# Performance work log

Hardware: AMD Instinct MI355X
Metric: run time of the kernel (lower is better)

The kernel has to match this reference:

```python
import jax, jax.numpy as jnp
import numpy as np

D_MODEL = 1024
NUM_HEADS = 16
D_K = D_MODEL // NUM_HEADS
SCALE = D_K ** 0.5


def setup_inputs() -> dict:
    key = jax.random.key(0)
    ks = jax.random.split(key, 11)
    B, S = 2, 2048
    std = 1.0 / np.sqrt(D_MODEL)
    inp = {
        "query": jax.random.normal(ks[0], (B, S, D_MODEL), dtype=jnp.float32),
        "key": jax.random.normal(ks[1], (B, S, D_MODEL), dtype=jnp.float32),
        "value": jax.random.normal(ks[2], (B, S, D_MODEL), dtype=jnp.float32),
        "wq": jax.random.uniform(ks[3], (D_MODEL, D_MODEL), jnp.float32, -std, std),
        "bq": jax.random.uniform(ks[4], (D_MODEL,), jnp.float32, -std, std),
        "wk": jax.random.uniform(ks[5], (D_MODEL, D_MODEL), jnp.float32, -std, std),
        "bk": jax.random.uniform(ks[6], (D_MODEL,), jnp.float32, -std, std),
        "wv": jax.random.uniform(ks[7], (D_MODEL, D_MODEL), jnp.float32, -std, std),
        "bv": jax.random.uniform(ks[8], (D_MODEL,), jnp.float32, -std, std),
        "wo": jax.random.uniform(ks[9], (D_MODEL, D_MODEL), jnp.float32, -std, std),
        "bo": jax.random.uniform(ks[10], (D_MODEL,), jnp.float32, -std, std),
    }
    return inp


def _split_heads(x):
    # [B, S, d_model] -> [B, H, S, d_k]
    B, S, _ = x.shape
    return x.reshape(B, S, NUM_HEADS, D_K).transpose(0, 2, 1, 3)


def reference(query, key, value, wq, bq, wk, bk, wv, bv, wo, bo):
    # Linear layers: torch Linear computes x @ W^T + b; weights here stored as [out, in]
    q = _split_heads(query @ wq.T + bq)  # [B, H, S, d_k]
    k = _split_heads(key @ wk.T + bk)
    v = _split_heads(value @ wv.T + bv)
    scores = jnp.einsum("bhqd,bhkd->bhqk", q, k) / SCALE  # [B, H, Sq, Sk]
    attn = jax.nn.softmax(scores, axis=-1)
    ctx = jnp.einsum("bhqk,bhkd->bhqd", attn, v)  # [B, H, S, d_k]
    B, H, S, dk = ctx.shape
    ctx = ctx.transpose(0, 2, 1, 3).reshape(B, S, D_MODEL)
    return ctx @ wo.T + bo
```

## Files before the change

### kernel.cpp

```cpp
#include <hip/hip_runtime.h>
#include <hip/hip_bf16.h>


typedef __attribute__((ext_vector_type(8))) short short8;
typedef __attribute__((ext_vector_type(4))) float floatx4;

#define D_MODEL 1024
#define SEQ 2048
#define NTOK 4096
#define DK 64
#define NH 16
#define MAT 4194304
#define WMAT 1048576

static __device__ __forceinline__ unsigned short f2bf(float f) {
    unsigned int x = __float_as_uint(f);
    unsigned int r = x + 0x7fffu + ((x >> 16) & 1u);
    return (unsigned short)(r >> 16);
}
static __device__ __forceinline__ float bf2f(unsigned short u) {
    return __uint_as_float(((unsigned int)u) << 16);
}
static __device__ __forceinline__ unsigned pk2(float x, float y) {
    __hip_bfloat162 h = __float22bfloat162_rn(make_float2(x, y));
    return *reinterpret_cast<unsigned*>(&h);
}
static __device__ __forceinline__ short8 cvt8(float4 f0, float4 f1) {
    union { unsigned u[4]; short8 s; } r;
    r.u[0] = pk2(f0.x, f0.y); r.u[1] = pk2(f0.z, f0.w);
    r.u[2] = pk2(f1.x, f1.y); r.u[3] = pk2(f1.z, f1.w);
    return r.s;
}

__global__ __launch_bounds__(256) void cvt7(
    const float* __restrict__ s0, const float* __restrict__ s1,
    const float* __restrict__ s2, const float* __restrict__ s3,
    const float* __restrict__ s4, const float* __restrict__ s5,
    const float* __restrict__ s6, unsigned short* __restrict__ dst) {
    const float* s; size_t doff; int n;
    switch (blockIdx.y) {
        case 0: s = s0; doff = 0;                          n = MAT;  break;
        case 1: s = s1; doff = (size_t)MAT;                n = MAT;  break;
        case 2: s = s2; doff = (size_t)2 * MAT;            n = MAT;  break;
        case 3: s = s3; doff = (size_t)3 * MAT;            n = WMAT; break;
        case 4: s = s4; doff = (size_t)3 * MAT + WMAT;     n = WMAT; break;
        case 5: s = s5; doff = (size_t)3 * MAT + 2 * WMAT; n = WMAT; break;
        default: s = s6; doff = (size_t)3 * MAT + 3 * WMAT; n = WMAT; break;
    }
    int idx = (blockIdx.x * 256 + threadIdx.x) * 8;
    if (idx >= n) return;
    float4 a = *(const float4*)(s + idx);
    float4 b = *(const float4*)(s + idx + 4);
    *(short8*)&dst[doff + idx] = cvt8(a, b);
}

template <bool F32OUT>
static __device__ __forceinline__ void gemm_bb(const unsigned short* __restrict__ X,
                                               const unsigned short* __restrict__ W,
                                               const float* __restrict__ bias,
                                               void* __restrict__ outp) {
    __shared__ __align__(16) unsigned short Asm[128 * 72];
    __shared__ __align__(16) unsigned short Bsm[128 * 72];

    const int tid = threadIdx.x;
    const int lane = tid & 63;
    const int wv = tid >> 6;
    const int g = lane >> 4;
    const int lm = lane & 15;
    const int wr = wv >> 1;
    const int wc = wv & 1;
    const int m0 = blockIdx.y * 128;
    const int n0 = blockIdx.x * 128;

    floatx4 acc[4][4];
#pragma unroll
    for (int mi = 0; mi < 4; ++mi)
#pragma unroll
        for (int ni = 0; ni < 4; ++ni)
            acc[mi][ni] = (floatx4){0.f, 0.f, 0.f, 0.f};

    for (int k0 = 0; k0 < 1024; k0 += 64) {
#pragma unroll
        for (int i = 0; i < 4; ++i) {
            int idx = tid + i * 256;
            int row = idx >> 3;
            int col = (idx & 7) << 3;
            *(uint4*)&Asm[row * 72 + col] =
                *(const uint4*)&X[(size_t)(m0 + row) * 1024 + k0 + col];
            *(uint4*)&Bsm[row * 72 + col] =
                *(const uint4*)&W[(size_t)(n0 + row) * 1024 + k0 + col];
        }
        __syncthreads();
#pragma unroll
        for (int ks = 0; ks < 64; ks += 32) {
            short8 af[4], bfr[4];
#pragma unroll
            for (int mi = 0; mi < 4; ++mi)
                af[mi] = *(const short8*)&Asm[(wr * 64 + mi * 16 + lm) * 72 + ks + g * 8];
#pragma unroll
            for (int ni = 0; ni < 4; ++ni)
                bfr[ni] = *(const short8*)&Bsm[(wc * 64 + ni * 16 + lm) * 72 + ks + g * 8];
#pragma unroll
            for (int mi = 0; mi < 4; ++mi)
#pragma unroll
                for (int ni = 0; ni < 4; ++ni)
                    acc[mi][ni] = __builtin_amdgcn_mfma_f32_16x16x32_bf16(
                        af[mi], bfr[ni], acc[mi][ni], 0, 0, 0);
        }
        __syncthreads();
    }

    float bb[4];
#pragma unroll
    for (int ni = 0; ni < 4; ++ni)
        bb[ni] = bias[n0 + wc * 64 + ni * 16 + lm];
#pragma unroll
    for (int mi = 0; mi < 4; ++mi)
#pragma unroll
        for (int ni = 0; ni < 4; ++ni)
#pragma unroll
            for (int r = 0; r < 4; ++r) {
                int rowg = m0 + wr * 64 + mi * 16 + g * 4 + r;
                int colg = n0 + wc * 64 + ni * 16 + lm;
                if (F32OUT)
                    ((float*)outp)[(size_t)rowg * 1024 + colg] = acc[mi][ni][r] + bb[ni];
                else
                    ((unsigned short*)outp)[(size_t)rowg * 1024 + colg] =
                        f2bf(acc[mi][ni][r] + bb[ni]);
            }
}

__global__ __launch_bounds__(256) void qkv_gemm_b(
    const unsigned short* __restrict__ Xb, const unsigned short* __restrict__ Wb,
    const float* __restrict__ bq, const float* __restrict__ bk,
    const float* __restrict__ bv, unsigned short* __restrict__ QKV) {
    const int z = blockIdx.z;
    const float* bias = (z == 0) ? bq : (z == 1) ? bk : bv;
    gemm_bb<false>(Xb + (size_t)z * MAT, Wb + (size_t)z * WMAT, bias,
                   QKV + (size_t)z * MAT);
}

__global__ __launch_bounds__(256) void out_gemm_b(
    const unsigned short* __restrict__ ctx, const unsigned short* __restrict__ Wo,
    const float* __restrict__ bo, float* __restrict__ out) {
    gemm_bb<true>(ctx, Wo, bo, out);
}

static __device__ __forceinline__ void gemm128_f(const float* __restrict__ X,
                                                 const float* __restrict__ W,
                                                 const float* __restrict__ bias,
                                                 unsigned short* __restrict__ out) {
    __shared__ __align__(16) unsigned short Asm[128 * 72];
    __shared__ __align__(16) unsigned short Bsm[128 * 72];
    const int tid = threadIdx.x;
    const int lane = tid & 63;
    const int wv = tid >> 6;
    const int g = lane >> 4;
    const int lm = lane & 15;
    const int wr = wv >> 1;
    const int wc = wv & 1;
    const int m0 = blockIdx.y * 128;
    const int n0 = blockIdx.x * 128;
    floatx4 acc[4][4];
#pragma unroll
    for (int mi = 0; mi < 4; ++mi)
#pragma unroll
        for (int ni = 0; ni < 4; ++ni)
            acc[mi][ni] = (floatx4){0.f, 0.f, 0.f, 0.f};
    for (int k0 = 0; k0 < 1024; k0 += 64) {
#pragma unroll
        for (int i = 0; i < 4; ++i) {
            int idx = tid + i * 256;
            int row = idx >> 3;
            int col = (idx & 7) << 3;
            const float* sa = &X[(size_t)(m0 + row) * 1024 + k0 + col];
            *(short8*)&Asm[row * 72 + col] = cvt8(*(const float4*)sa, *(const float4*)(sa + 4));
            const float* sb = &W[(size_t)(n0 + row) * 1024 + k0 + col];
            *(short8*)&Bsm[row * 72 + col] = cvt8(*(const float4*)sb, *(const float4*)(sb + 4));
        }
        __syncthreads();
#pragma unroll
        for (int ks = 0; ks < 64; ks += 32) {
            short8 af[4], bfr[4];
#pragma unroll
            for (int mi = 0; mi < 4; ++mi)
                af[mi] = *(const short8*)&Asm[(wr * 64 + mi * 16 + lm) * 72 + ks + g * 8];
#pragma unroll
            for (int ni = 0; ni < 4; ++ni)
                bfr[ni] = *(const short8*)&Bsm[(wc * 64 + ni * 16 + lm) * 72 + ks + g * 8];
#pragma unroll
            for (int mi = 0; mi < 4; ++mi)
#pragma unroll
                for (int ni = 0; ni < 4; ++ni)
                    acc[mi][ni] = __builtin_amdgcn_mfma_f32_16x16x32_bf16(
                        af[mi], bfr[ni], acc[mi][ni], 0, 0, 0);
        }
        __syncthreads();
    }
    float bb[4];
#pragma unroll
    for (int ni = 0; ni < 4; ++ni)
        bb[ni] = bias[n0 + wc * 64 + ni * 16 + lm];
#pragma unroll
    for (int mi = 0; mi < 4; ++mi)
#pragma unroll
        for (int ni = 0; ni < 4; ++ni)
#pragma unroll
            for (int r = 0; r < 4; ++r) {
                int rowg = m0 + wr * 64 + mi * 16 + g * 4 + r;
                int colg = n0 + wc * 64 + ni * 16 + lm;
                out[(size_t)rowg * 1024 + colg] = f2bf(acc[mi][ni][r] + bb[ni]);
            }
}

__global__ __launch_bounds__(256) void qkv_gemm_f(
    const float* __restrict__ xq, const float* __restrict__ xk,
    const float* __restrict__ xv, const float* __restrict__ wq,
    const float* __restrict__ wk, const float* __restrict__ wv,
    const float* __restrict__ bq, const float* __restrict__ bk,
    const float* __restrict__ bv, unsigned short* __restrict__ q,
    unsigned short* __restrict__ k, unsigned short* __restrict__ v) {
    const float *X, *W, *Bb;
    unsigned short* O;
    if (blockIdx.z == 0)      { X = xq; W = wq; Bb = bq; O = q; }
    else if (blockIdx.z == 1) { X = xk; W = wk; Bb = bk; O = k; }
    else                      { X = xv; W = wv; Bb = bv; O = v; }
    gemm128_f(X, W, Bb, O);
}

__global__ __launch_bounds__(256) void out_gemm_f(
    const float* __restrict__ wo, const float* __restrict__ bo,
    const unsigned short* __restrict__ ctx, float* __restrict__ out) {
    __shared__ __align__(16) unsigned short Asm[128 * 72];
    __shared__ __align__(16) unsigned short Bsm[128 * 72];
    const int tid = threadIdx.x;
    const int lane = tid & 63;
    const int wv = tid >> 6;
    const int g = lane >> 4;
    const int lm = lane & 15;
    const int wr = wv >> 1;
    const int wc = wv & 1;
    const int m0 = blockIdx.y * 128;
    const int n0 = blockIdx.x * 128;
    floatx4 acc[4][4];
#pragma unroll
    for (int mi = 0; mi < 4; ++mi)
#pragma unroll
        for (int ni = 0; ni < 4; ++ni)
            acc[mi][ni] = (floatx4){0.f, 0.f, 0.f, 0.f};
    for (int k0 = 0; k0 < 1024; k0 += 64) {
#pragma unroll
        for (int i = 0; i < 4; ++i) {
            int idx = tid + i * 256;
            int row = idx >> 3;
            int col = (idx & 7) << 3;
            *(uint4*)&Asm[row * 72 + col] =
                *(const uint4*)&ctx[(size_t)(m0 + row) * 1024 + k0 + col];
            const float* sb = &wo[(size_t)(n0 + row) * 1024 + k0 + col];
            *(short8*)&Bsm[row * 72 + col] = cvt8(*(const float4*)sb, *(const float4*)(sb + 4));
        }
        __syncthreads();
#pragma unroll
        for (int ks = 0; ks < 64; ks += 32) {
            short8 af[4], bfr[4];
#pragma unroll
            for (int mi = 0; mi < 4; ++mi)
                af[mi] = *(const short8*)&Asm[(wr * 64 + mi * 16 + lm) * 72 + ks + g * 8];
#pragma unroll
            for (int ni = 0; ni < 4; ++ni)
                bfr[ni] = *(const short8*)&Bsm[(wc * 64 + ni * 16 + lm) * 72 + ks + g * 8];
#pragma unroll
            for (int mi = 0; mi < 4; ++mi)
#pragma unroll
                for (int ni = 0; ni < 4; ++ni)
                    acc[mi][ni] = __builtin_amdgcn_mfma_f32_16x16x32_bf16(
                        af[mi], bfr[ni], acc[mi][ni], 0, 0, 0);
        }
        __syncthreads();
    }
    float bb[4];
#pragma unroll
    for (int ni = 0; ni < 4; ++ni)
        bb[ni] = bo[n0 + wc * 64 + ni * 16 + lm];
#pragma unroll
    for (int mi = 0; mi < 4; ++mi)
#pragma unroll
        for (int ni = 0; ni < 4; ++ni)
#pragma unroll
            for (int r = 0; r < 4; ++r) {
                int rowg = m0 + wr * 64 + mi * 16 + g * 4 + r;
                int colg = n0 + wc * 64 + ni * 16 + lm;
                out[(size_t)rowg * 1024 + colg] = acc[mi][ni][r] + bb[ni];
            }
}

__global__ __launch_bounds__(256) void attn_kernel(
    const unsigned short* __restrict__ Q, const unsigned short* __restrict__ K,
    const unsigned short* __restrict__ V, unsigned short* __restrict__ CTX) {
    __shared__ __align__(16) unsigned short Ksm[64 * 72];
    __shared__ __align__(16) unsigned short Vt[64 * 72];
    __shared__ __align__(16) unsigned short Psm[4 * 16 * 72];

    const int tid = threadIdx.x;
    const int lane = tid & 63;
    const int w = tid >> 6;
    const int g = lane >> 4;
    const int lm = lane & 15;
    const int qt = blockIdx.x;
    const int bh = blockIdx.y;
    const int b = bh >> 4;
    const int h = bh & 15;

    const size_t base = (size_t)b * SEQ * D_MODEL + (size_t)h * DK;

    short8 aq[2];
    const int qrow = qt * 64 + w * 16 + lm;
#pragma unroll
    for (int t = 0; t < 2; ++t) {
        short8 raw = *(const short8*)&Q[base + (size_t)qrow * D_MODEL + t * 32 + g * 8];
        union { unsigned u[4]; short8 s; } r;
#pragma unroll
        for (int j = 0; j < 4; ++j) {
            float lo = bf2f((unsigned short)raw[2 * j]) * 0.125f;
            float hi = bf2f((unsigned short)raw[2 * j + 1]) * 0.125f;
            r.u[j] = pk2(lo, hi);
        }
        aq[t] = r.s;
    }

    float lrow[4] = {0.f, 0.f, 0.f, 0.f};
    floatx4 Oacc[4];
#pragma unroll
    for (int nb = 0; nb < 4; ++nb) Oacc[nb] = (floatx4){0.f, 0.f, 0.f, 0.f};

    for (int kt = 0; kt < SEQ / 64; ++kt) {
        const int krow0 = kt * 64;
#pragma unroll
        for (int i = 0; i < 2; ++i) {
            int idx = tid + i * 256;
            int row = idx >> 3;
            int colb = (idx & 7) << 3;
            *(uint4*)&Ksm[row * 72 + colb] =
                *(const uint4*)&K[base + (size_t)(krow0 + row) * D_MODEL + colb];
            uint4 vv = *(const uint4*)&V[base + (size_t)(krow0 + row) * D_MODEL + colb];
            const unsigned short* vs = (const unsigned short*)&vv;
            int kcol = (row + ((colb >> 3) << 3)) & 63;
#pragma unroll
            for (int j = 0; j < 8; ++j)
                Vt[(colb + j) * 72 + kcol] = vs[j];
        }
        __syncthreads();

        floatx4 s[4];
#pragma unroll
        for (int nb = 0; nb < 4; ++nb) {
            floatx4 a = (floatx4){0.f, 0.f, 0.f, 0.f};
#pragma unroll
            for (int t = 0; t < 2; ++t) {
                short8 bk = *(const short8*)&Ksm[(nb * 16 + lm) * 72 + t * 32 + g * 8];
                a = __builtin_amdgcn_mfma_f32_16x16x32_bf16(aq[t], bk, a, 0, 0, 0);
            }
#pragma unroll
            for (int r = 0; r < 4; ++r) s[nb][r] = __expf(a[r]);
        }
#pragma unroll
        for (int r = 0; r < 4; ++r)
            lrow[r] += (s[0][r] + s[1][r]) + (s[2][r] + s[3][r]);

#pragma unroll
        for (int nb = 0; nb < 4; ++nb)
#pragma unroll
            for (int r = 0; r < 4; ++r) {
                int prow = w * 16 + g * 4 + r;
                Psm[prow * 72 + ((nb * 16 + lm + (g << 4)) & 63)] = f2bf(s[nb][r]);
            }

        short8 ap[2];
        const int prot = ((lm >> 2) & 3) << 4;
#pragma unroll
        for (int t = 0; t < 2; ++t)
            ap[t] = *(const short8*)&Psm[(w * 16 + lm) * 72 +
                                         ((t * 32 + g * 8 + prot) & 63)];
#pragma unroll
        for (int nb = 0; nb < 4; ++nb) {
            const int dk = nb * 16 + lm;
            const int sh = ((dk >> 3) & 7) << 3;
#pragma unroll
            for (int t = 0; t < 2; ++t) {
                int kcol = (t * 32 + g * 8 + sh) & 63;
                short8 bvv = *(const short8*)&Vt[dk * 72 + kcol];
                Oacc[nb] = __builtin_amdgcn_mfma_f32_16x16x32_bf16(ap[t], bvv, Oacc[nb], 0, 0, 0);
            }
        }
        __syncthreads();
    }

#pragma unroll
    for (int r = 0; r < 4; ++r)
#pragma unroll
        for (int off = 1; off < 16; off <<= 1)
            lrow[r] += __shfl_xor(lrow[r], off, 64);

#pragma unroll
    for (int nb = 0; nb < 4; ++nb) {
#pragma unroll
        for (int r = 0; r < 4; ++r) {
            float val = Oacc[nb][r] / lrow[r];
            int srow = qt * 64 + w * 16 + g * 4 + r;
            CTX[base + (size_t)srow * D_MODEL + nb * 16 + lm] = f2bf(val);
        }
    }
}

extern "C" void kernel_launch(void* const* d_in, const int* in_sizes, int n_in,
                              void* d_out, int out_size, void* d_ws, size_t ws_size,
                              hipStream_t stream) {
    const float* xq = (const float*)d_in[0];
    const float* xk = (const float*)d_in[1];
    const float* xv = (const float*)d_in[2];
    const float* wq = (const float*)d_in[3];
    const float* bq = (const float*)d_in[4];
    const float* wk = (const float*)d_in[5];
    const float* bk = (const float*)d_in[6];
    const float* wv = (const float*)d_in[7];
    const float* bv = (const float*)d_in[8];
    const float* wo = (const float*)d_in[9];
    const float* bo = (const float*)d_in[10];
    float* out = (float*)d_out;

    unsigned short* ws = (unsigned short*)d_ws;

    if (ws_size >= (size_t)68 * 1024 * 1024) {
        unsigned short* Xb = ws;
        unsigned short* Wb = ws + (size_t)3 * MAT;
        unsigned short* Qw = Wb + (size_t)4 * WMAT;
        unsigned short* Kw = Qw + (size_t)MAT;
        unsigned short* Vw = Kw + (size_t)MAT;
        unsigned short* Cw = Vw + (size_t)MAT;

        cvt7<<<dim3(2048, 7), 256, 0, stream>>>(xq, xk, xv, wq, wk, wv, wo, ws);
        qkv_gemm_b<<<dim3(8, 32, 3), 256, 0, stream>>>(Xb, Wb, bq, bk, bv, Qw);
        attn_kernel<<<dim3(SEQ / 64, 2 * NH), 256, 0, stream>>>(Qw, Kw, Vw, Cw);
        out_gemm_b<<<dim3(8, 32), 256, 0, stream>>>(Cw, Wb + (size_t)3 * WMAT, bo, out);
    } else {
        unsigned short* Qw = ws;
        unsigned short* Kw = ws + (size_t)MAT;
        unsigned short* Vw = ws + (size_t)2 * MAT;
        unsigned short* Cw = ws + (size_t)3 * MAT;
        qkv_gemm_f<<<dim3(8, 32, 3), 256, 0, stream>>>(
            xq, xk, xv, wq, wk, wv, bq, bk, bv, Qw, Kw, Vw);
        attn_kernel<<<dim3(SEQ / 64, 2 * NH), 256, 0, stream>>>(Qw, Kw, Vw, Cw);
        out_gemm_f<<<dim3(8, 32), 256, 0, stream>>>(wo, bo, Cw, out);
    }
}
```

Measured before the change: 273.6 us.

## Compute transposed scores so P feeds PV MFMA from registers, drop Psm

The QK^T MFMA now computes S^T (K as A operand, Q as B), so each lane holds scores for a single query row across key positions, which lets the exponentiated probabilities be packed directly into the A-operand layout of the PV MFMA without a round trip through shared memory. The Psm buffer and its scattered stores and loads are removed, and the row-sum reduction becomes a single per-lane sum plus two shuffles. V is now transposed into shared memory with 32-bit gathers across four key rows and 64-bit stores, and the Vt read pattern is matched to the new key ordering. The V global loads become narrower, 4-byte strided accesses, which may reduce load efficiency.

Result: slower. 324.9 us (+18.7%).

```diff
diff --git a/kernel.cpp b/kernel.cpp
--- a/kernel.cpp
+++ b/kernel.cpp
@@ -299,7 +299,6 @@
     const unsigned short* __restrict__ V, unsigned short* __restrict__ CTX) {
     __shared__ __align__(16) unsigned short Ksm[64 * 72];
     __shared__ __align__(16) unsigned short Vt[64 * 72];
-    __shared__ __align__(16) unsigned short Psm[4 * 16 * 72];
 
     const int tid = threadIdx.x;
     const int lane = tid & 63;
@@ -313,7 +312,7 @@
 
     const size_t base = (size_t)b * SEQ * D_MODEL + (size_t)h * DK;
 
-    short8 aq[2];
+    short8 qf[2];
     const int qrow = qt * 64 + w * 16 + lm;
 #pragma unroll
     for (int t = 0; t < 2; ++t) {
@@ -325,10 +324,10 @@
             float hi = bf2f((unsigned short)raw[2 * j + 1]) * 0.125f;
             r.u[j] = pk2(lo, hi);
         }
-        aq[t] = r.s;
-    }
-
-    float lrow[4] = {0.f, 0.f, 0.f, 0.f};
+        qf[t] = r.s;
+    }
+
+    float lsum = 0.f;
     floatx4 Oacc[4];
 #pragma unroll
     for (int nb = 0; nb < 4; ++nb) Oacc[nb] = (floatx4){0.f, 0.f, 0.f, 0.f};
@@ -342,70 +341,72 @@
             int colb = (idx & 7) << 3;
             *(uint4*)&Ksm[row * 72 + colb] =
                 *(const uint4*)&K[base + (size_t)(krow0 + row) * D_MODEL + colb];
-            uint4 vv = *(const uint4*)&V[base + (size_t)(krow0 + row) * D_MODEL + colb];
-            const unsigned short* vs = (const unsigned short*)&vv;
-            int kcol = (row + ((colb >> 3) << 3)) & 63;
-#pragma unroll
-            for (int j = 0; j < 8; ++j)
-                Vt[(colb + j) * 72 + kcol] = vs[j];
-        }
-        __syncthreads();
-
-        floatx4 s[4];
-#pragma unroll
-        for (int nb = 0; nb < 4; ++nb) {
+
+            int dp = idx >> 4;
+            int kq = idx & 15;
+            const unsigned* vsrc =
+                (const unsigned*)&V[base + (size_t)(krow0 + 4 * kq) * D_MODEL + 2 * dp];
+            unsigned w0 = vsrc[0];
+            unsigned w1 = vsrc[512];
+            unsigned w2 = vsrc[1024];
+            unsigned w3 = vsrc[1536];
+            unsigned lo0 = (w0 & 0xffffu) | (w1 << 16);
+            unsigned lo1 = (w2 & 0xffffu) | (w3 << 16);
+            unsigned hi0 = (w0 >> 16) | (w1 & 0xffff0000u);
+            unsigned hi1 = (w2 >> 16) | (w3 & 0xffff0000u);
+            *(uint2*)&Vt[(2 * dp) * 72 + 4 * kq] = make_uint2(lo0, lo1);
+            *(uint2*)&Vt[(2 * dp + 1) * 72 + 4 * kq] = make_uint2(hi0, hi1);
+        }
+        __syncthreads();
+
+        float p[4][4];
+#pragma unroll
+        for (int kb = 0; kb < 4; ++kb) {
             floatx4 a = (floatx4){0.f, 0.f, 0.f, 0.f};
 #pragma unroll
             for (int t = 0; t < 2; ++t) {
-                short8 bk = *(const short8*)&Ksm[(nb * 16 + lm) * 72 + t * 32 + g * 8];
-                a = __builtin_amdgcn_mfma_f32_16x16x32_bf16(aq[t], bk, a, 0, 0, 0);
+                short8 ak = *(const short8*)&Ksm[(kb * 16 + lm) * 72 + t * 32 + g * 8];
+                a = __builtin_amdgcn_mfma_f32_16x16x32_bf16(ak, qf[t], a, 0, 0, 0);
             }
 #pragma unroll
-            for (int r = 0; r < 4; ++r) s[nb][r] = __expf(a[r]);
-        }
-#pragma unroll
-        for (int r = 0; r < 4; ++r)
-            lrow[r] += (s[0][r] + s[1][r]) + (s[2][r] + s[3][r]);
-
-#pragma unroll
-        for (int nb = 0; nb < 4; ++nb)
-#pragma unroll
-            for (int r = 0; r < 4; ++r) {
-                int prow = w * 16 + g * 4 + r;
-                Psm[prow * 72 + ((nb * 16 + lm + (g << 4)) & 63)] = f2bf(s[nb][r]);
+            for (int r = 0; r < 4; ++r) p[kb][r] = __expf(a[r]);
+            lsum += (p[kb][0] + p[kb][1]) + (p[kb][2] + p[kb][3]);
+        }
+
+#pragma unroll
+        for (int cp = 0; cp < 2; ++cp) {
+            const int c0 = 2 * cp, c1 = 2 * cp + 1;
+            union { unsigned u[4]; short8 s; } ap;
+            ap.u[0] = pk2(p[c0][0], p[c0][1]);
+            ap.u[1] = pk2(p[c0][2], p[c0][3]);
+            ap.u[2] = pk2(p[c1][0], p[c1][1]);
+            ap.u[3] = pk2(p[c1][2], p[c1][3]);
+#pragma unroll
+            for (int nb = 0; nb < 4; ++nb) {
+                const int d = nb * 16 + lm;
+                uint2 x0 = *(const uint2*)&Vt[d * 72 + c0 * 16 + g * 4];
+                uint2 x1 = *(const uint2*)&Vt[d * 72 + c1 * 16 + g * 4];
+                union { unsigned u[4]; short8 s; } bv;
+                bv.u[0] = x0.x; bv.u[1] = x0.y; bv.u[2] = x1.x; bv.u[3] = x1.y;
+                Oacc[nb] = __builtin_amdgcn_mfma_f32_16x16x32_bf16(
+                    ap.s, bv.s, Oacc[nb], 0, 0, 0);
             }
-
-        short8 ap[2];
-        const int prot = ((lm >> 2) & 3) << 4;
-#pragma unroll
-        for (int t = 0; t < 2; ++t)
-            ap[t] = *(const short8*)&Psm[(w * 16 + lm) * 72 +
-                                         ((t * 32 + g * 8 + prot) & 63)];
-#pragma unroll
-        for (int nb = 0; nb < 4; ++nb) {
-            const int dk = nb * 16 + lm;
-            const int sh = ((dk >> 3) & 7) << 3;
-#pragma unroll
-            for (int t = 0; t < 2; ++t) {
-                int kcol = (t * 32 + g * 8 + sh) & 63;
-                short8 bvv = *(const short8*)&Vt[dk * 72 + kcol];
-                Oacc[nb] = __builtin_amdgcn_mfma_f32_16x16x32_bf16(ap[t], bvv, Oacc[nb], 0, 0, 0);
-            }
-        }
-        __syncthreads();
-    }
-
+        }
+        __syncthreads();
+    }
+
+    lsum += __shfl_xor(lsum, 16, 64);
+    lsum += __shfl_xor(lsum, 32, 64);
+    float lr[4];
 #pragma unroll
     for (int r = 0; r < 4; ++r)
-#pragma unroll
-        for (int off = 1; off < 16; off <<= 1)
-            lrow[r] += __shfl_xor(lrow[r], off, 64);
+        lr[r] = __shfl(lsum, g * 4 + r, 64);
 
 #pragma unroll
     for (int nb = 0; nb < 4; ++nb) {
 #pragma unroll
         for (int r = 0; r < 4; ++r) {
-            float val = Oacc[nb][r] / lrow[r];
+            float val = Oacc[nb][r] / lr[r];
             int srow = qt * 64 + w * 16 + g * 4 + r;
             CTX[base + (size_t)srow * D_MODEL + nb * 16 + lm] = f2bf(val);
         }
```
